# Kernel optimization log

Hardware: AMD Instinct MI355X
Metric: run time of the kernel (lower is better)

Reference implementation:

```python
import jax, jax.numpy as jnp
import numpy as np

FSIZE = 5
PAD = FSIZE // 2


def _conv(mosaick, filts):
    # mosaick [B,1,H,W], filts [f,f,K] -> responses [B,K,H,W].
    # Cross-correlation with edge-clamped boundary (Halide clamp semantics).
    x = jnp.pad(mosaick, ((0, 0), (0, 0), (PAD, PAD), (PAD, PAD)), mode='edge')
    k = jnp.transpose(filts, (2, 0, 1))[:, None, :, :]  # [K,1,f,f] OIHW
    return jax.lax.conv_general_dilated(
        x, k, window_strides=(1, 1), padding='VALID',
        dimension_numbers=('NCHW', 'OIHW', 'NCHW'))


def setup_inputs() -> dict:
    key = jax.random.key(0)
    k1, k2, k3 = jax.random.split(key, 3)
    B, H, W, K, f = 16, 512, 512, 8, FSIZE
    std = 1.0 / (f * f)  # matches normal_(0, 1/(fsize*fsize))
    return {
        'mosaick': jax.random.normal(k1, (B, 1, H, W), dtype=jnp.float32),
        'sel_filts': jax.random.normal(k2, (f, f, K), dtype=jnp.float32) * std,
        'green_filts': jax.random.normal(k3, (f, f, K), dtype=jnp.float32) * std,
    }


def reference(mosaick, sel_filts, green_filts):
    # Per-pixel soft filter selection over K candidate green-interpolation filters.
    sel = _conv(mosaick, sel_filts)      # [B,K,H,W] selection scores
    grn = _conv(mosaick, green_filts)    # [B,K,H,W] candidate green estimates
    w = jax.nn.softmax(sel, axis=1)      # softmax over filter bank
    interp = jnp.sum(w * grn, axis=1, keepdims=True)  # [B,1,H,W]
    # GRBG Bayer: green where row parity == col parity; copy known greens.
    H, W = mosaick.shape[-2], mosaick.shape[-1]
    yy = jnp.arange(H)[:, None]
    xx = jnp.arange(W)[None, :]
    is_green = (yy % 2) == (xx % 2)      # [H,W] bool
    # Output green channel only (module returns output[:, 1:2, ...]).
    return jnp.where(is_green, mosaick, interp)
```

## Files before the change

kernel.cpp:

```cpp
#include <hip/hip_runtime.h>


typedef float v2f __attribute__((ext_vector_type(2)));

#define BDIM 256
#define TW 64
#define TH 32
#define LWT (TW + 4)
#define LHT (TH + 4)

__global__ __launch_bounds__(BDIM, 4) void demosaick_kernel(
    const float* __restrict__ mos,
    const float* __restrict__ sf,
    const float* __restrict__ gf,
    float* __restrict__ out,
    int H, int W)
{
    __shared__ float tile[LHT * LWT];

    const int tid   = threadIdx.x;
    const int b     = blockIdx.z;
    const int tileX = blockIdx.x * TW;
    const int tileY = blockIdx.y * TH;
    const float* img = mos + (size_t)b * H * W;

    for (int i = tid; i < LHT * LWT; i += BDIM) {
        int r = i / LWT;
        int c = i - r * LWT;
        int gy = min(max(tileY - 2 + r, 0), H - 1);
        int gx = min(max(tileX - 2 + c, 0), W - 1);
        tile[i] = img[(size_t)gy * W + gx];
    }
    __syncthreads();

    const int lane = tid & 63;
    const int g    = tid >> 6;
    const int xc   = tileX + lane;
    const int p    = xc & 1;
    const int lx   = lane + 2;
    const int y0   = tileY + g * 8;

    v2f acc[4][8];
#pragma unroll
    for (int r = 0; r < 4; ++r)
#pragma unroll
        for (int j = 0; j < 8; ++j) acc[r][j] = (v2f)(0.f);

    const int rowbase = g * 8 + 1 - p;

#pragma unroll
    for (int dx = 0; dx < 5; ++dx) {
        const int cx = lx + dx - 2;
        float cache[11];
#pragma unroll
        for (int i = 0; i < 11; ++i)
            cache[i] = tile[(rowbase + i) * LWT + cx];
#pragma unroll
        for (int dy = 0; dy < 5; ++dy) {
            const float* fsp = sf + (dy * 5 + dx) * 8;
            const float* fgp = gf + (dy * 5 + dx) * 8;
            v2f f[8];
            f[0] = *(const v2f*)(fsp);
            f[1] = *(const v2f*)(fsp + 2);
            f[2] = *(const v2f*)(fsp + 4);
            f[3] = *(const v2f*)(fsp + 6);
            f[4] = *(const v2f*)(fgp);
            f[5] = *(const v2f*)(fgp + 2);
            f[6] = *(const v2f*)(fgp + 4);
            f[7] = *(const v2f*)(fgp + 6);
#pragma unroll
            for (int r = 0; r < 4; ++r) {
                const float v = cache[2 * r + dy];
                const v2f vv = { v, v };
#pragma unroll
                for (int j = 0; j < 8; ++j)
                    acc[r][j] = __builtin_elementwise_fma(vv, f[j], acc[r][j]);
            }
        }
    }

    const size_t ob = (size_t)b * H * W;
#pragma unroll
    for (int r = 0; r < 4; ++r) {
        float s[8], gr[8];
#pragma unroll
        for (int j = 0; j < 4; ++j) {
            s[2 * j]      = acc[r][j].x;
            s[2 * j + 1]  = acc[r][j].y;
            gr[2 * j]     = acc[r][4 + j].x;
            gr[2 * j + 1] = acc[r][4 + j].y;
        }
        float m = s[0];
#pragma unroll
        for (int k = 1; k < 8; ++k) m = fmaxf(m, s[k]);
        float num = 0.f, den = 0.f;
#pragma unroll
        for (int k = 0; k < 8; ++k) {
            float e = __expf(s[k] - m);
            num = fmaf(e, gr[k], num);
            den += e;
        }
        const float interp = num / den;
        const float green  = tile[(g * 8 + 2 * r + p + 2) * LWT + lx];
        out[ob + (size_t)(y0 + 2 * r + p) * W + xc]     = green;
        out[ob + (size_t)(y0 + 2 * r + 1 - p) * W + xc] = interp;
    }
}

extern "C" void kernel_launch(void* const* d_in, const int* in_sizes, int n_in,
                              void* d_out, int out_size, void* d_ws, size_t ws_size,
                              hipStream_t stream) {
    const float* mos = (const float*)d_in[0];
    const float* sf  = (const float*)d_in[1];
    const float* gf  = (const float*)d_in[2];
    float* out = (float*)d_out;

    const int H = 512, W = 512;
    const int B = in_sizes[0] / (H * W);

    dim3 grid(W / TW, H / TH, B);
    dim3 block(BDIM);
    demosaick_kernel<<<grid, block, 0, stream>>>(mos, sf, gf, out, H, W);
}
```

Before: 92.39 us.

## Shrink tile to one non-green pixel per thread, vectorize interior loads

Tile height drops from 32 to 8, so each thread computes one 2-row Bayer pair (one interpolated pixel) instead of four. This cuts accumulator registers sharply and launches four times as many blocks for occupancy. Interior tiles load their halo with float2 loads and no clamping, and H/W become compile-time constants. In exchange, the halo-to-output ratio rises (12 rows loaded per 8 output rows) and filter reuse per thread drops.

Result: slower. 98.23 us (+6.3%).

```diff
diff --git a/kernel.cpp b/kernel.cpp
--- a/kernel.cpp
+++ b/kernel.cpp
@@ -5,7 +5,7 @@
 
 #define BDIM 256
 #define TW 64
-#define TH 32
+#define TH 8
 #define LWT (TW + 4)
 #define LHT (TH + 4)
 
@@ -13,48 +13,63 @@
     const float* __restrict__ mos,
     const float* __restrict__ sf,
     const float* __restrict__ gf,
-    float* __restrict__ out,
-    int H, int W)
+    float* __restrict__ out)
 {
+    const int H = 512, W = 512;
     __shared__ float tile[LHT * LWT];
 
     const int tid   = threadIdx.x;
+    const int bx    = blockIdx.x;
+    const int by    = blockIdx.y;
     const int b     = blockIdx.z;
-    const int tileX = blockIdx.x * TW;
-    const int tileY = blockIdx.y * TH;
+    const int tileX = bx * TW;
+    const int sy    = by * TH;
     const float* img = mos + (size_t)b * H * W;
 
-    for (int i = tid; i < LHT * LWT; i += BDIM) {
-        int r = i / LWT;
-        int c = i - r * LWT;
-        int gy = min(max(tileY - 2 + r, 0), H - 1);
-        int gx = min(max(tileX - 2 + c, 0), W - 1);
-        tile[i] = img[(size_t)gy * W + gx];
+    const bool interior = (bx > 0) && (bx < gridDim.x - 1) &&
+                          (by > 0) && (by < gridDim.y - 1);
+
+    if (interior) {
+#pragma unroll
+        for (int it = 0; it < 2; ++it) {
+            int i = tid + it * BDIM;
+            if (i < 408) {
+                int r  = i / 34;
+                int c2 = i - r * 34;
+                const float2 v = *(const float2*)(img + (size_t)(sy - 2 + r) * W
+                                                  + (tileX - 2 + 2 * c2));
+                *(float2*)&tile[r * LWT + 2 * c2] = v;
+            }
+        }
+    } else {
+        for (int i = tid; i < LHT * LWT; i += BDIM) {
+            int r = i / LWT;
+            int c = i - r * LWT;
+            int gy = min(max(sy - 2 + r, 0), H - 1);
+            int gx = min(max(tileX - 2 + c, 0), W - 1);
+            tile[i] = img[(size_t)gy * W + gx];
+        }
     }
     __syncthreads();
 
     const int lane = tid & 63;
     const int g    = tid >> 6;
     const int xc   = tileX + lane;
-    const int p    = xc & 1;
-    const int lx   = lane + 2;
-    const int y0   = tileY + g * 8;
+    const int p    = lane & 1;
+    const int lc   = 2 + 2 * g + 1 - p;
+    const int lg   = 2 + 2 * g + p;
 
-    v2f acc[4][8];
+    v2f acc[8];
 #pragma unroll
-    for (int r = 0; r < 4; ++r)
-#pragma unroll
-        for (int j = 0; j < 8; ++j) acc[r][j] = (v2f)(0.f);
-
-    const int rowbase = g * 8 + 1 - p;
+    for (int j = 0; j < 8; ++j) acc[j] = (v2f)(0.f);
 
 #pragma unroll
     for (int dx = 0; dx < 5; ++dx) {
-        const int cx = lx + dx - 2;
-        float cache[11];
+        const int cx = lane + dx;
+        float cache[5];
 #pragma unroll
-        for (int i = 0; i < 11; ++i)
-            cache[i] = tile[(rowbase + i) * LWT + cx];
+        for (int i = 0; i < 5; ++i)
+            cache[i] = tile[(lc - 2 + i) * LWT + cx];
 #pragma unroll
         for (int dy = 0; dy < 5; ++dy) {
             const float* fsp = sf + (dy * 5 + dx) * 8;
@@ -68,43 +83,35 @@
             f[5] = *(const v2f*)(fgp + 2);
             f[6] = *(const v2f*)(fgp + 4);
             f[7] = *(const v2f*)(fgp + 6);
+            const float v = cache[dy];
+            const v2f vv = { v, v };
 #pragma unroll
-            for (int r = 0; r < 4; ++r) {
-                const float v = cache[2 * r + dy];
-                const v2f vv = { v, v };
-#pragma unroll
-                for (int j = 0; j < 8; ++j)
-                    acc[r][j] = __builtin_elementwise_fma(vv, f[j], acc[r][j]);
-            }
+            for (int j = 0; j < 8; ++j)
+                acc[j] = __builtin_elementwise_fma(vv, f[j], acc[j]);
         }
     }
 
-    const size_t ob = (size_t)b * H * W;
+    v2f m2 = __builtin_elementwise_max(
+                 __builtin_elementwise_max(acc[0], acc[1]),
+                 __builtin_elementwise_max(acc[2], acc[3]));
+    const float m = fmaxf(m2.x, m2.y);
+    v2f num2 = (v2f)(0.f), den2 = (v2f)(0.f);
 #pragma unroll
-    for (int r = 0; r < 4; ++r) {
-        float s[8], gr[8];
-#pragma unroll
-        for (int j = 0; j < 4; ++j) {
-            s[2 * j]      = acc[r][j].x;
-            s[2 * j + 1]  = acc[r][j].y;
-            gr[2 * j]     = acc[r][4 + j].x;
-            gr[2 * j + 1] = acc[r][4 + j].y;
-        }
-        float m = s[0];
-#pragma unroll
-        for (int k = 1; k < 8; ++k) m = fmaxf(m, s[k]);
-        float num = 0.f, den = 0.f;
-#pragma unroll
-        for (int k = 0; k < 8; ++k) {
-            float e = __expf(s[k] - m);
-            num = fmaf(e, gr[k], num);
-            den += e;
-        }
-        const float interp = num / den;
-        const float green  = tile[(g * 8 + 2 * r + p + 2) * LWT + lx];
-        out[ob + (size_t)(y0 + 2 * r + p) * W + xc]     = green;
-        out[ob + (size_t)(y0 + 2 * r + 1 - p) * W + xc] = interp;
+    for (int j = 0; j < 4; ++j) {
+        v2f e;
+        e.x = __expf(acc[j].x - m);
+        e.y = __expf(acc[j].y - m);
+        den2 += e;
+        num2 = __builtin_elementwise_fma(e, acc[4 + j], num2);
     }
+    const float num = num2.x + num2.y;
+    const float den = den2.x + den2.y;
+    const float interp = num / den;
+    const float green  = tile[lg * LWT + lane + 2];
+
+    float* op = out + (size_t)b * H * W + (size_t)(sy + 2 * g) * W + xc;
+    op[(size_t)p * W]       = green;
+    op[(size_t)(1 - p) * W] = interp;
 }
 
 extern "C" void kernel_launch(void* const* d_in, const int* in_sizes, int n_in,
@@ -120,5 +127,5 @@
 
     dim3 grid(W / TW, H / TH, B);
     dim3 block(BDIM);
-    demosaick_kernel<<<grid, block, 0, stream>>>(mos, sf, gf, out, H, W);
+    demosaick_kernel<<<grid, block, 0, stream>>>(mos, sf, gf, out);
 }
```
